# Kernel tuning notes

Hardware: AMD Instinct MI355X
Metric: run time of the kernel (lower is better)

The kernel has to match this reference:

```python
import jax, jax.numpy as jnp
import numpy as np

N = 50000      # num nodes
E = 800000     # num edges (avg degree 16)
H = 128        # hidden_dim
D = 3          # node_dim (decoder output)
L = 4          # num_layers


def setup_inputs() -> dict:
    key = jax.random.key(0)
    ks = jax.random.split(key, 6)
    s = 0.05
    x = jax.random.normal(ks[0], (N, H), dtype=jnp.float32)
    edge_index = jax.random.randint(ks[1], (2, E), 0, N, dtype=jnp.int64)
    # per-layer EdgeConv MLP params: Linear(2H->H), ReLU, Linear(H->H)
    W1 = jax.random.normal(ks[2], (L, 2 * H, H), dtype=jnp.float32) * s
    b1 = jnp.zeros((L, H), dtype=jnp.float32)
    W2 = jax.random.normal(ks[3], (L, H, H), dtype=jnp.float32) * s
    b2 = jnp.zeros((L, H), dtype=jnp.float32)
    # final fc: Linear(H -> D)
    Wf = jax.random.normal(ks[4], (H, D), dtype=jnp.float32) * s
    bf = jnp.zeros((D,), dtype=jnp.float32)
    return {"x": x, "edge_index": edge_index, "W1": W1, "b1": b1,
            "W2": W2, "b2": b2, "Wf": Wf, "bf": bf}


def reference(x, edge_index, W1, b1, W2, b2, Wf, bf):
    n = x.shape[0]
    # add_self_loops: every node has at least one incoming message
    loops = jnp.arange(n, dtype=edge_index.dtype)
    src = jnp.concatenate([edge_index[0], loops])  # x_j source
    dst = jnp.concatenate([edge_index[1], loops])  # x_i target / aggregate index
    for l in range(W1.shape[0]):
        x_i = x[dst]                                   # [E+N, H] gather targets
        x_j = x[src]                                   # [E+N, H] gather sources
        msg = jnp.concatenate([x_i, x_j - x_i], axis=-1)   # [E+N, 2H]
        msg = jax.nn.relu(msg @ W1[l] + b1[l]) @ W2[l] + b2[l]  # edge MLP
        x = jax.ops.segment_max(msg, dst, num_segments=n)       # max aggregate
    return x @ Wf + bf  # [N, D]
```

## Files before the change

### kernel.cpp

```cpp
#include <hip/hip_runtime.h>
#include <hip/hip_fp16.h>

typedef _Float16 f16;
typedef _Float16 f16x8 __attribute__((ext_vector_type(8)));
typedef __fp16 hf16x2 __attribute__((ext_vector_type(2)));
typedef float f32x4 __attribute__((ext_vector_type(4)));
typedef float f32x2 __attribute__((ext_vector_type(2)));
typedef unsigned int u32;
typedef u32 u32x4 __attribute__((ext_vector_type(4)));

#define HDIM 128
#define LAYERS 4
#define TS 32
#define NEG_BIG (-3.0e38f)

static __device__ __forceinline__ f32x4 mfma16(f16x8 a, f16x8 b, f32x4 c) {
  return __builtin_amdgcn_mfma_f32_16x16x32_f16(a, b, c, 0, 0, 0);
}

static __device__ __forceinline__ void atomicMaxF(float* addr, float val) {
  if (val >= 0.f) atomicMax((int*)addr, __float_as_int(val));
  else            atomicMin((unsigned int*)addr, __float_as_uint(val));
}

static __device__ __forceinline__ f16x8 pack4(hf16x2 a, hf16x2 b, hf16x2 c, hf16x2 d) {
  u32x4 u = {__builtin_bit_cast(u32, a), __builtin_bit_cast(u32, b),
             __builtin_bit_cast(u32, c), __builtin_bit_cast(u32, d)};
  return __builtin_bit_cast(f16x8, u);
}

static __device__ __forceinline__ void split8(f32x4 a, f32x4 b, f16x8& hv, f16x8& lv) {
  hf16x2 h0 = __builtin_amdgcn_cvt_pkrtz(a.x, a.y);
  hf16x2 h1 = __builtin_amdgcn_cvt_pkrtz(a.z, a.w);
  hf16x2 h2 = __builtin_amdgcn_cvt_pkrtz(b.x, b.y);
  hf16x2 h3 = __builtin_amdgcn_cvt_pkrtz(b.z, b.w);
  hv = pack4(h0, h1, h2, h3);
  hf16x2 l0 = __builtin_amdgcn_cvt_pkrtz(a.x - (float)h0[0], a.y - (float)h0[1]);
  hf16x2 l1 = __builtin_amdgcn_cvt_pkrtz(a.z - (float)h1[0], a.w - (float)h1[1]);
  hf16x2 l2 = __builtin_amdgcn_cvt_pkrtz(b.x - (float)h2[0], b.y - (float)h2[1]);
  hf16x2 l3 = __builtin_amdgcn_cvt_pkrtz(b.z - (float)h3[0], b.w - (float)h3[1]);
  lv = pack4(l0, l1, l2, l3);
}

__global__ void gnn_hist(const int* __restrict__ ei, int* __restrict__ deg, int E) {
  int e = blockIdx.x * 256 + threadIdx.x;
  if (e < E) atomicAdd(&deg[ei[E + e]], 1);
}

__global__ void gnn_bsum(const int* __restrict__ deg, int* __restrict__ bsum, int N) {
  __shared__ int red[256];
  int v = blockIdx.x * 256 + threadIdx.x;
  red[threadIdx.x] = (v < N) ? (deg[v] + 1) : 0;
  __syncthreads();
  for (int d = 128; d; d >>= 1) {
    if (threadIdx.x < d) red[threadIdx.x] += red[threadIdx.x + d];
    __syncthreads();
  }
  if (threadIdx.x == 0) bsum[blockIdx.x] = red[0];
}

__global__ void gnn_bscan(const int* __restrict__ bsum, int* __restrict__ boffs,
                          int* __restrict__ offs, int nb, int N) {
  __shared__ int sh[256];
  int t = threadIdx.x;
  sh[t] = (t < nb) ? bsum[t] : 0;
  __syncthreads();
  for (int d = 1; d < 256; d <<= 1) {
    int add = (t >= d) ? sh[t - d] : 0;
    __syncthreads();
    sh[t] += add;
    __syncthreads();
  }
  boffs[t] = (t > 0) ? sh[t - 1] : 0;
  if (t == 255) offs[N] = sh[255];
}

__global__ void gnn_scan_fin(const int* __restrict__ deg, const int* __restrict__ boffs,
                             int* __restrict__ offs, int* __restrict__ cursor,
                             int* __restrict__ colsrc, int* __restrict__ nodeof, int N) {
  __shared__ int sh[256];
  int t = threadIdx.x;
  int v = blockIdx.x * 256 + t;
  int val = (v < N) ? (deg[v] + 1) : 0;
  sh[t] = val;
  __syncthreads();
  for (int d = 1; d < 256; d <<= 1) {
    int add = (t >= d) ? sh[t - d] : 0;
    __syncthreads();
    sh[t] += add;
    __syncthreads();
  }
  if (v < N) {
    int excl = boffs[blockIdx.x] + sh[t] - val;
    offs[v] = excl;
    cursor[v] = excl + 1;
    colsrc[excl] = v;
    int e = excl + val;
    for (int s = excl; s < e; s++) nodeof[s] = v;
  }
}

__global__ void gnn_scatter(const int* __restrict__ ei, int* __restrict__ cursor,
                            int* __restrict__ colsrc, int E) {
  int e = blockIdx.x * 256 + threadIdx.x;
  if (e < E) {
    int d = ei[E + e];
    int p = atomicAdd(&cursor[d], 1);
    colsrc[p] = ei[e];
  }
}

__global__ void gnn_biasprep(const float* __restrict__ W1, const float* __restrict__ b1,
                             const float* __restrict__ b2, const float* __restrict__ Wf,
                             const float* __restrict__ bf, float* __restrict__ cbias,
                             float* __restrict__ bfp) {
  int l = blockIdx.x, c = threadIdx.x;
  if (l < LAYERS) {
    float s = 0.f;
    if (l > 0) {
      const float* bp = b2 + (size_t)(l - 1) * HDIM;
      if (c < 128) {
        for (int k = 0; k < 128; k++)
          s += bp[k] * (W1[((size_t)l * 256 + k) * 128 + c] - W1[((size_t)l * 256 + 128 + k) * 128 + c]);
      } else {
        int cc = c - 128;
        for (int k = 0; k < 128; k++)
          s += bp[k] * W1[((size_t)l * 256 + 128 + k) * 128 + cc];
      }
    }
    float base = (c < 128) ? b1[(size_t)l * HDIM + c] : 0.f;
    cbias[l * 256 + c] = base + s;
  } else if (c < 3) {
    float s = bf[c];
    for (int k = 0; k < 128; k++) s += b2[3 * HDIM + k] * Wf[k * 3 + c];
    bfp[c] = s;
  }
}

__global__ void gnn_wprep1(const float* __restrict__ W1, f16* __restrict__ Wc) {
  int id = blockIdx.x * 256 + threadIdx.x;
  if (id >= LAYERS * 128 * 256) return;
  int col = id & 255, k = (id >> 8) & 127, l = id >> 15;
  float w;
  if (col < 128) w = W1[((size_t)l * 256 + k) * 128 + col] - W1[((size_t)l * 256 + 128 + k) * 128 + col];
  else           w = W1[((size_t)l * 256 + 128 + k) * 128 + (col - 128)];
  f16 hi = (f16)w;
  f16 lo = (f16)(w - (float)hi);
  int kk = k >> 5, quad = (k >> 3) & 3, j = k & 7;
  int ntile = col >> 4, lane = quad * 16 + (col & 15);
  size_t base = ((((size_t)l * 2 + 0) * 4 + kk) * 16 + ntile) * 512 + lane * 8 + j;
  Wc[base] = hi;
  Wc[base + (size_t)4 * 16 * 512] = lo;
}

__global__ void gnn_wprep2(const float* __restrict__ W2, f16* __restrict__ W2f) {
  int id = blockIdx.x * 256 + threadIdx.x;
  if (id >= LAYERS * 128 * 128) return;
  int n = id & 127, k = (id >> 7) & 127, l = id >> 14;
  float w = W2[((size_t)l * 128 + k) * 128 + n];
  f16 hi = (f16)w;
  f16 lo = (f16)(w - (float)hi);
  int kk = k >> 5, quad = (k >> 3) & 3, j = k & 7;
  int ntile = n >> 4, lane = quad * 16 + (n & 15);
  size_t base = ((((size_t)l * 2 + 0) * 4 + kk) * 8 + ntile) * 512 + lane * 8 + j;
  W2f[base] = hi;
  W2f[base + (size_t)4 * 8 * 512] = lo;
}

__global__ __launch_bounds__(256) void gnn_pq(const float* __restrict__ x,
    const f16* __restrict__ Wc, const float* __restrict__ cbias,
    float* __restrict__ P, float* __restrict__ Q, int N,
    const int* __restrict__ offs, int spb, float* __restrict__ xinit) {
  __shared__ __align__(16) f16 shA[2 * 4 * 4 * 64 * 8];
  int tid = threadIdx.x;
  int row0 = blockIdx.x * 64;
#pragma unroll
  for (int i = 0; i < 4; i++) {
    int p = i * 256 + tid;
    int row = p & 63, seg = p >> 6;
    f32x4 a = {}, b = {};
    int gr = row0 + row;
    if (gr < N) {
      const f32x4* xp = (const f32x4*)(x + (size_t)gr * HDIM + seg * 8);
      a = xp[0]; b = xp[1];
    }
    f16x8 hv, lv;
    split8(a, b, hv, lv);
    int kk = seg >> 2, quad = seg & 3, mt = row >> 4, m = row & 15;
    int lane = quad * 16 + m;
    int off = ((kk * 4 + mt) * 64 + lane) * 8;
    *(f16x8*)&shA[off] = hv;
    *(f16x8*)&shA[off + 4 * 4 * 64 * 8] = lv;
  }
  __syncthreads();
  int wave = tid >> 6, lane = tid & 63;
  int quad = lane >> 4, cl = lane & 15;
  f16x8 bw[2][4][4];
#pragma unroll
  for (int pl = 0; pl < 2; pl++)
#pragma unroll
    for (int nt = 0; nt < 4; nt++)
#pragma unroll
      for (int kk = 0; kk < 4; kk++) {
        int ntile = wave * 4 + nt;
        bw[pl][nt][kk] = *(const f16x8*)&Wc[(((size_t)(pl * 4 + kk) * 16 + ntile) * 64 + lane) * 8];
      }
#pragma unroll
  for (int mt = 0; mt < 4; mt++) {
    f32x4 acc[4] = {};
#pragma unroll
    for (int kk = 0; kk < 4; kk++) {
      f16x8 ah = *(const f16x8*)&shA[((kk * 4 + mt) * 64 + lane) * 8];
      f16x8 al = *(const f16x8*)&shA[(((4 + kk) * 4 + mt) * 64 + lane) * 8];
#pragma unroll
      for (int nt = 0; nt < 4; nt++) {
        acc[nt] = mfma16(ah, bw[0][nt][kk], acc[nt]);
        acc[nt] = mfma16(al, bw[0][nt][kk], acc[nt]);
        acc[nt] = mfma16(ah, bw[1][nt][kk], acc[nt]);
      }
    }
#pragma unroll
    for (int nt = 0; nt < 4; nt++) {
      int c = (wave * 4 + nt) * 16 + cl;
      float bb = cbias[c];
      float* dst = (c < HDIM) ? P : Q;
      int cc = c & 127;
#pragma unroll
      for (int i = 0; i < 4; i++) {
        int gr = row0 + mt * 16 + quad * 4 + i;
        if (gr < N) dst[(size_t)gr * HDIM + cc] = acc[nt][i] + bb;
      }
    }
  }
  if (tid < 64) {
    int v = row0 + tid;
    if (v < N) {
      int a = offs[v], b = offs[v + 1] - 1;
      if (a / spb != b / spb) {
        f32x4 ninf = {NEG_BIG, NEG_BIG, NEG_BIG, NEG_BIG};
        float* xr = xinit + (size_t)v * HDIM;
#pragma unroll
        for (int c = 0; c < HDIM; c += 4) *(f32x4*)(xr + c) = ninf;
      }
    }
  }
}

__global__ __launch_bounds__(256, 4) void gnn_edge6(
    const float* __restrict__ P, const float* __restrict__ Q,
    const int* __restrict__ offs, const int* __restrict__ colsrc,
    const int* __restrict__ nodeof, const f16* __restrict__ W2f,
    float* __restrict__ xout, int S, int spb) {
  __shared__ __align__(16) f16 shA[2 * 4 * 2 * 64 * 8];
  __shared__ __align__(16) float msg[TS * 132];
  __shared__ __align__(16) float stradV[2][128];
  __shared__ int stradN[2];
  int tid = threadIdx.x;
  int wave = tid >> 6, lane = tid & 63;
  int quad = lane >> 4, cl = lane & 15;
  f16x8 bw[2][2][4];
#pragma unroll
  for (int pl = 0; pl < 2; pl++)
#pragma unroll
    for (int nt = 0; nt < 2; nt++)
#pragma unroll
      for (int kk = 0; kk < 4; kk++)
        bw[pl][nt][kk] = *(const f16x8*)&W2f[(((size_t)(pl * 4 + kk) * 8 + (wave * 2 + nt)) * 64 + lane) * 8];
  int blk0 = blockIdx.x * spb;
  int blk1 = blk0 + spb; if (blk1 > S) blk1 = S;
  if (tid < 2) stradN[tid] = -1;
  int sl = tid >> 4, seg = tid & 15;
  int kkb = seg >> 2, qb = seg & 3;
  int laneF = qb * 16 + sl;
  int Sm1 = S - 1;
  int tc = 0;
  for (int t0 = blk0; t0 < blk1; t0 += TS, tc++) {
    int par = tc & 1, prv = par ^ 1;
    int tEnd = t0 + TS; if (tEnd > blk1) tEnd = blk1;
#pragma unroll
    for (int i = 0; i < 2; i++) {
      int slot = t0 + i * 16 + sl;
      int slc = (slot < S) ? slot : Sm1;
      int src = colsrc[slc];
      int dst = nodeof[slc];
      const f32x4* qp = (const f32x4*)(Q + (size_t)src * HDIM + seg * 8);
      const f32x4* pp = (const f32x4*)(P + (size_t)dst * HDIM + seg * 8);
      f32x4 qa = qp[0], qb4 = qp[1], pa = pp[0], pb = pp[1];
      f32x4 sa, sb;
      sa.x = fmaxf(pa.x + qa.x, 0.f); sa.y = fmaxf(pa.y + qa.y, 0.f);
      sa.z = fmaxf(pa.z + qa.z, 0.f); sa.w = fmaxf(pa.w + qa.w, 0.f);
      sb.x = fmaxf(pb.x + qb4.x, 0.f); sb.y = fmaxf(pb.y + qb4.y, 0.f);
      sb.z = fmaxf(pb.z + qb4.z, 0.f); sb.w = fmaxf(pb.w + qb4.w, 0.f);
      f16x8 hv, lv;
      split8(sa, sb, hv, lv);
      int off = ((kkb * 2 + i) * 64 + laneF) * 8;
      *(f16x8*)&shA[off] = hv;
      *(f16x8*)&shA[off + 4096] = lv;
    }
    __syncthreads();
    if (tid == 0) stradN[par] = -1;
    f32x4 acc[2][2] = {};
#pragma unroll
    for (int kk = 0; kk < 4; kk++)
#pragma unroll
      for (int mt = 0; mt < 2; mt++) {
        int off = ((kk * 2 + mt) * 64 + lane) * 8;
        f16x8 ah = *(const f16x8*)&shA[off];
        f16x8 al = *(const f16x8*)&shA[off + 4096];
#pragma unroll
        for (int nt = 0; nt < 2; nt++) {
          acc[mt][nt] = mfma16(ah, bw[0][nt][kk], acc[mt][nt]);
          acc[mt][nt] = mfma16(al, bw[0][nt][kk], acc[mt][nt]);
          acc[mt][nt] = mfma16(ah, bw[1][nt][kk], acc[mt][nt]);
        }
      }
#pragma unroll
    for (int mt = 0; mt < 2; mt++)
#pragma unroll
      for (int nt = 0; nt < 2; nt++) {
        int col = wave * 32 + nt * 16 + cl;
#pragma unroll
        for (int i = 0; i < 4; i++) {
          int row = mt * 16 + quad * 4 + i;
          msg[row * 132 + col] = acc[mt][nt][i];
        }
      }
    __syncthreads();
    int vA = nodeof[t0];
    int vB = nodeof[tEnd - 1];
    int sNp = stradN[prv];
    int ngroups = (vB - vA + 1) << 5;
    for (int p = tid; p < ngroups; p += 256) {
      int v = vA + (p >> 5), c4 = (p & 31) << 2;
      int a = offs[v], b = offs[v + 1];
      int r0 = (a > t0 ? a : t0) - t0;
      int r1 = (b < tEnd ? b : tEnd) - t0;
      f32x4 m = {NEG_BIG, NEG_BIG, NEG_BIG, NEG_BIG};
      for (int r = r0; r < r1; r++) {
        f32x4 x = *(const f32x4*)&msg[r * 132 + c4];
        m.x = fmaxf(m.x, x.x); m.y = fmaxf(m.y, x.y);
        m.z = fmaxf(m.z, x.z); m.w = fmaxf(m.w, x.w);
      }
      if (v == sNp) {
        f32x4 sv = *(const f32x4*)&stradV[prv][c4];
        m.x = fmaxf(m.x, sv.x); m.y = fmaxf(m.y, sv.y);
        m.z = fmaxf(m.z, sv.z); m.w = fmaxf(m.w, sv.w);
      }
      if (b > tEnd && tEnd < blk1) {
        *(f32x4*)&stradV[par][c4] = m;
        if ((p & 31) == 0) stradN[par] = v;
      } else {
        float* dp = &xout[(size_t)v * HDIM + c4];
        if (a < blk0 || b > blk1) {
          atomicMaxF(dp + 0, m.x); atomicMaxF(dp + 1, m.y);
          atomicMaxF(dp + 2, m.z); atomicMaxF(dp + 3, m.w);
        } else {
          *(f32x4*)dp = m;
        }
      }
    }
  }
}

__global__ __launch_bounds__(256) void gnn_fc(const float* __restrict__ x,
    const float* __restrict__ Wf, const float* __restrict__ bfp,
    float* __restrict__ out, int N) {
  int wave = threadIdx.x >> 6, lane = threadIdx.x & 63;
  int wid = blockIdx.x * 4 + wave, nw = gridDim.x * 4;
  int k0 = lane * 2;
  float w00 = Wf[k0 * 3 + 0], w01 = Wf[k0 * 3 + 1], w02 = Wf[k0 * 3 + 2];
  float w10 = Wf[k0 * 3 + 3], w11 = Wf[k0 * 3 + 4], w12 = Wf[k0 * 3 + 5];
  float bf0 = bfp[0], bf1 = bfp[1], bf2 = bfp[2];
  for (int v = wid; v < N; v += nw) {
    f32x2 xx = *(const f32x2*)(x + (size_t)v * HDIM + k0);
    float d0 = xx.x * w00 + xx.y * w10;
    float d1 = xx.x * w01 + xx.y * w11;
    float d2 = xx.x * w02 + xx.y * w12;
#pragma unroll
    for (int s = 32; s; s >>= 1) {
      d0 += __shfl_xor(d0, s, 64);
      d1 += __shfl_xor(d1, s, 64);
      d2 += __shfl_xor(d2, s, 64);
    }
    if (lane == 0) {
      out[(size_t)v * 3 + 0] = d0 + bf0;
      out[(size_t)v * 3 + 1] = d1 + bf1;
      out[(size_t)v * 3 + 2] = d2 + bf2;
    }
  }
}

extern "C" void kernel_launch(void* const* d_in, const int* in_sizes, int n_in,
                              void* d_out, int out_size, void* d_ws, size_t ws_size,
                              hipStream_t stream) {
  const float* x_in = (const float*)d_in[0];
  const int*   ei   = (const int*)d_in[1];
  const float* W1   = (const float*)d_in[2];
  const float* b1   = (const float*)d_in[3];
  const float* W2   = (const float*)d_in[4];
  const float* b2   = (const float*)d_in[5];
  const float* Wf   = (const float*)d_in[6];
  const float* bfv  = (const float*)d_in[7];
  float* outp = (float*)d_out;
  int N = in_sizes[0] / HDIM;
  int E = in_sizes[1] / 2;
  int S = E + N;

  char* ws = (char*)d_ws;
  size_t o = 0;
  auto alloc = [&](size_t bytes) -> char* {
    char* p = ws + o;
    o += (bytes + 255) & ~(size_t)255;
    return p;
  };
  int*   deg    = (int*)alloc((size_t)N * 4);
  int*   offs   = (int*)alloc(((size_t)N + 1) * 4);
  int*   cursor = (int*)alloc((size_t)N * 4);
  int*   colsrc = (int*)alloc((size_t)S * 4);
  int*   nodeof = (int*)alloc((size_t)S * 4);
  int*   bsum   = (int*)alloc(256 * 4);
  int*   boffs  = (int*)alloc(256 * 4);
  float* cbias  = (float*)alloc((size_t)LAYERS * 256 * 4);
  float* bfp    = (float*)alloc(4 * 4);
  float* P      = (float*)alloc((size_t)N * HDIM * 4);
  float* Q      = (float*)alloc((size_t)N * HDIM * 4);
  float* xbuf   = (float*)alloc((size_t)N * HDIM * 4);
  f16*   Wc     = (f16*)alloc((size_t)LAYERS * 65536 * 2);
  f16*   W2f    = (f16*)alloc((size_t)LAYERS * 32768 * 2);
  (void)ws_size; (void)n_in; (void)out_size;

  int nb = (N + 255) / 256;
  hipMemsetAsync(deg, 0, (size_t)N * 4, stream);
  gnn_hist<<<(E + 255) / 256, 256, 0, stream>>>(ei, deg, E);
  gnn_bsum<<<nb, 256, 0, stream>>>(deg, bsum, N);
  gnn_bscan<<<1, 256, 0, stream>>>(bsum, boffs, offs, nb, N);
  gnn_scan_fin<<<nb, 256, 0, stream>>>(deg, boffs, offs, cursor, colsrc, nodeof, N);
  gnn_scatter<<<(E + 255) / 256, 256, 0, stream>>>(ei, cursor, colsrc, E);
  gnn_biasprep<<<LAYERS + 1, 256, 0, stream>>>(W1, b1, b2, Wf, bfv, cbias, bfp);
  gnn_wprep1<<<(LAYERS * 128 * 256 + 255) / 256, 256, 0, stream>>>(W1, Wc);
  gnn_wprep2<<<(LAYERS * 128 * 128 + 255) / 256, 256, 0, stream>>>(W2, W2f);

  int spb = ((((S + 1023) / 1024) + TS - 1) / TS) * TS;
  int NB = (S + spb - 1) / spb;
  const float* xc = x_in;
  for (int l = 0; l < LAYERS; l++) {
    gnn_pq<<<(N + 63) / 64, 256, 0, stream>>>(xc, Wc + (size_t)l * 65536, cbias + l * 256,
                                              P, Q, N, offs, spb, xbuf);
    gnn_edge6<<<NB, 256, 0, stream>>>(P, Q, offs, colsrc, nodeof, W2f + (size_t)l * 32768,
                                      xbuf, S, spb);
    xc = xbuf;
  }
  gnn_fc<<<256, 256, 0, stream>>>(xc, Wf, bfp, outp, N);
}
```

Before: 830.8 us.

## Reduce edge messages in registers with wave shuffles instead of LDS staging

The edge kernel no longer writes the MFMA accumulator tile to a shared-memory message buffer. Each wave instead loops over the destination nodes in the tile, masks rows outside the node's range, and reduces within the wave using xor shuffles. The freed LDS allows a launch bound of 6 blocks per SM and a grid of about 1536 blocks. nodeof filling moves from a serial per-node loop in the scan into the scatter kernel. In exchange, every wave now iterates serially over all nodes in the tile with shuffles on each step, which adds work when a tile spans many nodes.

```diff
diff --git a/kernel.cpp b/kernel.cpp
--- a/kernel.cpp
+++ b/kernel.cpp
@@ -95,18 +95,18 @@
     offs[v] = excl;
     cursor[v] = excl + 1;
     colsrc[excl] = v;
-    int e = excl + val;
-    for (int s = excl; s < e; s++) nodeof[s] = v;
+    nodeof[excl] = v;
   }
 }
 
 __global__ void gnn_scatter(const int* __restrict__ ei, int* __restrict__ cursor,
-                            int* __restrict__ colsrc, int E) {
+                            int* __restrict__ colsrc, int* __restrict__ nodeof, int E) {
   int e = blockIdx.x * 256 + threadIdx.x;
   if (e < E) {
     int d = ei[E + e];
     int p = atomicAdd(&cursor[d], 1);
     colsrc[p] = ei[e];
+    nodeof[p] = d;
   }
 }
 
@@ -246,13 +246,12 @@
   }
 }
 
-__global__ __launch_bounds__(256, 4) void gnn_edge6(
+__global__ __launch_bounds__(256, 6) void gnn_edge7(
     const float* __restrict__ P, const float* __restrict__ Q,
     const int* __restrict__ offs, const int* __restrict__ colsrc,
     const int* __restrict__ nodeof, const f16* __restrict__ W2f,
     float* __restrict__ xout, int S, int spb) {
   __shared__ __align__(16) f16 shA[2 * 4 * 2 * 64 * 8];
-  __shared__ __align__(16) float msg[TS * 132];
   __shared__ __align__(16) float stradV[2][128];
   __shared__ int stradN[2];
   int tid = threadIdx.x;
@@ -269,6 +268,7 @@
   int blk0 = blockIdx.x * spb;
   int blk1 = blk0 + spb; if (blk1 > S) blk1 = S;
   if (tid < 2) stradN[tid] = -1;
+  __syncthreads();
   int sl = tid >> 4, seg = tid & 15;
   int kkb = seg >> 2, qb = seg & 3;
   int laneF = qb * 16 + sl;
@@ -298,7 +298,6 @@
       *(f16x8*)&shA[off + 4096] = lv;
     }
     __syncthreads();
-    if (tid == 0) stradN[par] = -1;
     f32x4 acc[2][2] = {};
 #pragma unroll
     for (int kk = 0; kk < 4; kk++)
@@ -314,49 +313,49 @@
           acc[mt][nt] = mfma16(ah, bw[1][nt][kk], acc[mt][nt]);
         }
       }
-#pragma unroll
-    for (int mt = 0; mt < 2; mt++)
-#pragma unroll
-      for (int nt = 0; nt < 2; nt++) {
-        int col = wave * 32 + nt * 16 + cl;
-#pragma unroll
-        for (int i = 0; i < 4; i++) {
-          int row = mt * 16 + quad * 4 + i;
-          msg[row * 132 + col] = acc[mt][nt][i];
-        }
-      }
     __syncthreads();
     int vA = nodeof[t0];
     int vB = nodeof[tEnd - 1];
     int sNp = stradN[prv];
-    int ngroups = (vB - vA + 1) << 5;
-    for (int p = tid; p < ngroups; p += 256) {
-      int v = vA + (p >> 5), c4 = (p & 31) << 2;
+    for (int v = vA; v <= vB; v++) {
       int a = offs[v], b = offs[v + 1];
       int r0 = (a > t0 ? a : t0) - t0;
       int r1 = (b < tEnd ? b : tEnd) - t0;
-      f32x4 m = {NEG_BIG, NEG_BIG, NEG_BIG, NEG_BIG};
-      for (int r = r0; r < r1; r++) {
-        f32x4 x = *(const f32x4*)&msg[r * 132 + c4];
-        m.x = fmaxf(m.x, x.x); m.y = fmaxf(m.y, x.y);
-        m.z = fmaxf(m.z, x.z); m.w = fmaxf(m.w, x.w);
-      }
-      if (v == sNp) {
-        f32x4 sv = *(const f32x4*)&stradV[prv][c4];
-        m.x = fmaxf(m.x, sv.x); m.y = fmaxf(m.y, sv.y);
-        m.z = fmaxf(m.z, sv.z); m.w = fmaxf(m.w, sv.w);
-      }
-      if (b > tEnd && tEnd < blk1) {
-        *(f32x4*)&stradV[par][c4] = m;
-        if ((p & 31) == 0) stradN[par] = v;
-      } else {
-        float* dp = &xout[(size_t)v * HDIM + c4];
-        if (a < blk0 || b > blk1) {
-          atomicMaxF(dp + 0, m.x); atomicMaxF(dp + 1, m.y);
-          atomicMaxF(dp + 2, m.z); atomicMaxF(dp + 3, m.w);
+      float m0 = NEG_BIG, m1 = NEG_BIG;
+#pragma unroll
+      for (int mt = 0; mt < 2; mt++)
+#pragma unroll
+        for (int i = 0; i < 4; i++) {
+          int row = mt * 16 + quad * 4 + i;
+          bool in = (row >= r0) && (row < r1);
+          m0 = fmaxf(m0, in ? acc[mt][0][i] : NEG_BIG);
+          m1 = fmaxf(m1, in ? acc[mt][1][i] : NEG_BIG);
+        }
+      m0 = fmaxf(m0, __shfl_xor(m0, 16, 64));
+      m0 = fmaxf(m0, __shfl_xor(m0, 32, 64));
+      m1 = fmaxf(m1, __shfl_xor(m1, 16, 64));
+      m1 = fmaxf(m1, __shfl_xor(m1, 32, 64));
+      if (quad == 0) {
+        int col0 = wave * 32 + cl, col1 = col0 + 16;
+        if (v == sNp) {
+          m0 = fmaxf(m0, stradV[prv][col0]);
+          m1 = fmaxf(m1, stradV[prv][col1]);
+        }
+        bool carry = (b > tEnd) && (tEnd < blk1);
+        if (carry) {
+          stradV[par][col0] = m0;
+          stradV[par][col1] = m1;
         } else {
-          *(f32x4*)dp = m;
+          float* dp = &xout[(size_t)v * HDIM];
+          if (a < blk0 || b > blk1) {
+            atomicMaxF(dp + col0, m0);
+            atomicMaxF(dp + col1, m1);
+          } else {
+            dp[col0] = m0;
+            dp[col1] = m1;
+          }
         }
+        if (wave == 0 && cl == 0 && v == vB) stradN[par] = carry ? v : -1;
       }
     }
   }
@@ -435,18 +434,18 @@
   gnn_bsum<<<nb, 256, 0, stream>>>(deg, bsum, N);
   gnn_bscan<<<1, 256, 0, stream>>>(bsum, boffs, offs, nb, N);
   gnn_scan_fin<<<nb, 256, 0, stream>>>(deg, boffs, offs, cursor, colsrc, nodeof, N);
-  gnn_scatter<<<(E + 255) / 256, 256, 0, stream>>>(ei, cursor, colsrc, E);
+  gnn_scatter<<<(E + 255) / 256, 256, 0, stream>>>(ei, cursor, colsrc, nodeof, E);
   gnn_biasprep<<<LAYERS + 1, 256, 0, stream>>>(W1, b1, b2, Wf, bfv, cbias, bfp);
   gnn_wprep1<<<(LAYERS * 128 * 256 + 255) / 256, 256, 0, stream>>>(W1, Wc);
   gnn_wprep2<<<(LAYERS * 128 * 128 + 255) / 256, 256, 0, stream>>>(W2, W2f);
 
-  int spb = ((((S + 1023) / 1024) + TS - 1) / TS) * TS;
+  int spb = ((((S + 1535) / 1536) + TS - 1) / TS) * TS;
   int NB = (S + spb - 1) / spb;
   const float* xc = x_in;
   for (int l = 0; l < LAYERS; l++) {
     gnn_pq<<<(N + 63) / 64, 256, 0, stream>>>(xc, Wc + (size_t)l * 65536, cbias + l * 256,
                                               P, Q, N, offs, spb, xbuf);
-    gnn_edge6<<<NB, 256, 0, stream>>>(P, Q, offs, colsrc, nodeof, W2f + (size_t)l * 32768,
+    gnn_edge7<<<NB, 256, 0, stream>>>(P, Q, offs, colsrc, nodeof, W2f + (size_t)l * 32768,
                                       xbuf, S, spb);
     xc = xbuf;
   }
```

Result: slower. 1.250 ms (+50.5%).
